# Kernel optimization log

Hardware: AMD Instinct MI355X
Metric: run time of the kernel (lower is better)

## Reference

```python
import jax, jax.numpy as jnp
import numpy as np

T, N, F, H = 8, 2048, 128, 4  # seq_len, max_nodes, hidden_dim, num_heads


def setup_inputs() -> dict:
    key = jax.random.key(0)
    k1, k2 = jax.random.split(key)
    x = jax.random.normal(k1, (T, N, F), dtype=jnp.float32)
    # xavier_uniform with gain 1.414 over (hidden_dim, hidden_dim) fan
    limit = 1.414 * np.sqrt(6.0 / (F + F))
    W = jax.random.uniform(k2, (H, F, F), dtype=jnp.float32, minval=-limit, maxval=limit)
    return {"x": x, "W": W}


def reference(x, W):
    # x: [T, N, F] padded node embeddings (all timesteps full -> mask all True)
    # W: [H, F, F] per-head projection
    seq_len = x.shape[0]
    th = jnp.einsum('tnf,hfg->htng', x, W)          # [H, T, N, F] transformed
    q = th[:, -1]                                    # [H, N, F] query = last timestep (faithful to source loop structure)
    scores = jnp.einsum('hnf,htmf->htnm', q, th)     # [H, T, N, N]
    attn = jax.nn.softmax(scores, axis=-1)           # softmax over key nodes per (head, t2)
    s = jnp.einsum('htnm,htmf->hnf', attn, th)       # sum over t2 of attn @ transformed[t2]
    s = s / seq_len                                  # mean over the seq axis (only last slot filled)
    out = jax.nn.elu(s)                              # [H, N, F]
    return out.mean(axis=0)                          # mean over heads -> [N, F]
```

## Files before the change

kernel.cpp:

```cpp
#include <hip/hip_runtime.h>
#include <hip/hip_bf16.h>
#include <math.h>

#define T_ 8
#define N_ 2048
#define F_ 128
#define H_ 4
#define NT_ (N_ / 32)

typedef unsigned int u32;
typedef unsigned short ushort_t;
typedef float f32x16 __attribute__((ext_vector_type(16)));
typedef _Float16 f16x8 __attribute__((ext_vector_type(8)));
typedef u32 u32x4 __attribute__((ext_vector_type(4)));

__global__ __launch_bounds__(256) void k_th(const float* __restrict__ x,
                                            const float* __restrict__ W,
                                            ushort_t* __restrict__ th_hi,
                                            ushort_t* __restrict__ th_hiT) {
    const int b = blockIdx.x;
    const int h = b / (T_ * (N_ / 64));
    const int rem = b % (T_ * (N_ / 64));
    const int t = rem / (N_ / 64);
    const int n0 = (rem % (N_ / 64)) * 64;
    const int tid = threadIdx.x;
    const int lane = tid & 63;
    const int w = tid >> 6;
    const int l31 = lane & 31;
    const int h5 = lane >> 5;
    const int rh = w & 1;
    const int gh = w >> 1;

    f16x8 xh[8], xl[8];
    {
        const float* xrow = x + ((size_t)t * N_ + (n0 + rh * 32 + l31)) * F_ + h5 * 8;
        #pragma unroll
        for (int ks = 0; ks < 8; ++ks) {
            float4 v0 = *reinterpret_cast<const float4*>(xrow + ks * 16);
            float4 v1 = *reinterpret_cast<const float4*>(xrow + ks * 16 + 4);
            float vv[8] = {v0.x, v0.y, v0.z, v0.w, v1.x, v1.y, v1.z, v1.w};
            f16x8 hi, lo;
            #pragma unroll
            for (int j = 0; j < 8; ++j) {
                _Float16 hh = (_Float16)vv[j];
                hi[j] = hh;
                lo[j] = (_Float16)(vv[j] - (float)hh);
            }
            xh[ks] = hi; xl[ks] = lo;
        }
    }

    f16x8 wb0[8], wb1[8];
    {
        const float* Wb = W + (size_t)h * F_ * F_ + gh * 64 + 2 * l31;
        #pragma unroll
        for (int ks = 0; ks < 8; ++ks) {
            f16x8 b0, b1;
            #pragma unroll
            for (int j = 0; j < 8; ++j) {
                float2 wv = *reinterpret_cast<const float2*>(
                    Wb + (size_t)(ks * 16 + h5 * 8 + j) * F_);
                b0[j] = (_Float16)wv.x;
                b1[j] = (_Float16)wv.y;
            }
            wb0[ks] = b0; wb1[ks] = b1;
        }
    }

    f32x16 acc0, acc1;
    #pragma unroll
    for (int r = 0; r < 16; ++r) { acc0[r] = 0.f; acc1[r] = 0.f; }
    #pragma unroll
    for (int ks = 0; ks < 8; ++ks) {
        acc0 = __builtin_amdgcn_mfma_f32_32x32x16_f16(xh[ks], wb0[ks], acc0, 0, 0, 0);
        acc1 = __builtin_amdgcn_mfma_f32_32x32x16_f16(xh[ks], wb1[ks], acc1, 0, 0, 0);
        acc0 = __builtin_amdgcn_mfma_f32_32x32x16_f16(xl[ks], wb0[ks], acc0, 0, 0, 0);
        acc1 = __builtin_amdgcn_mfma_f32_32x32x16_f16(xl[ks], wb1[ks], acc1, 0, 0, 0);
    }

    const size_t ht = (size_t)h * T_ + t;

    {
        ushort_t* base = th_hi + (ht * N_ + (size_t)(n0 + rh * 32)) * F_ + gh * 64 + 2 * l31;
        #pragma unroll
        for (int reg = 0; reg < 16; ++reg) {
            const int r = (reg & 3) + 8 * (reg >> 2) + 4 * h5;
            auto r2 = __builtin_amdgcn_cvt_pkrtz(acc0[reg], acc1[reg]);
            *reinterpret_cast<u32*>(base + (size_t)r * F_) = __builtin_bit_cast(u32, r2);
        }
    }

    {
        const int nc = (n0 >> 5) + rh;
        #pragma unroll
        for (int gs = 0; gs < 2; ++gs) {
            const int g = gh * 64 + 2 * l31 + gs;
            const f32x16& A = gs ? acc1 : acc0;
            ushort_t* bg = th_hiT + ((ht * (N_ / 32) + nc) * F_ + g) * 32;
            u32x4 run0, run1;
            run0.x = __builtin_bit_cast(u32, __builtin_amdgcn_cvt_pkrtz(A[0], A[1]));
            run0.y = __builtin_bit_cast(u32, __builtin_amdgcn_cvt_pkrtz(A[2], A[3]));
            run0.z = __builtin_bit_cast(u32, __builtin_amdgcn_cvt_pkrtz(A[4], A[5]));
            run0.w = __builtin_bit_cast(u32, __builtin_amdgcn_cvt_pkrtz(A[6], A[7]));
            run1.x = __builtin_bit_cast(u32, __builtin_amdgcn_cvt_pkrtz(A[8], A[9]));
            run1.y = __builtin_bit_cast(u32, __builtin_amdgcn_cvt_pkrtz(A[10], A[11]));
            run1.z = __builtin_bit_cast(u32, __builtin_amdgcn_cvt_pkrtz(A[12], A[13]));
            run1.w = __builtin_bit_cast(u32, __builtin_amdgcn_cvt_pkrtz(A[14], A[15]));
            *reinterpret_cast<u32x4*>(bg + 8 * h5) = run0;
            *reinterpret_cast<u32x4*>(bg + 16 + 8 * h5) = run1;
        }
    }
}

__global__ __launch_bounds__(256, 2) void k_attn(const ushort_t* __restrict__ th_hi,
                                                 const ushort_t* __restrict__ th_hiT,
                                                 ushort_t* __restrict__ s_part) {
    __shared__ ushort_t kh[3][32][128];
    __shared__ ushort_t vt[4][64][72];

    const int tid = threadIdx.x;
    const int lane = tid & 63;
    const int w = tid >> 6;
    const int l31 = lane & 31;
    const int h5 = lane >> 5;

    const int vid = ((blockIdx.x & 7) << 6) | (blockIdx.x >> 3);
    const int h = vid >> 7;
    const int t = (vid >> 4) & 7;
    const int qt = vid & 15;
    const int q0 = qt * 128 + w * 32;

    const size_t ht = (size_t)h * T_ + t;
    const ushort_t* Khi_g = th_hi + ht * (N_ * F_);
    const ushort_t* VT_g  = th_hiT + ht * ((N_ / 32) * F_ * 32);
    const ushort_t* Qhi_g = th_hi + ((size_t)h * T_ + (T_ - 1)) * (N_ * F_);

    f16x8 qh[8];
    {
        const _Float16 L2E = (_Float16)1.4426950408889634f;
        const ushort_t* qrh = Qhi_g + (size_t)(q0 + l31) * F_ + h5 * 8;
        #pragma unroll
        for (int ks = 0; ks < 8; ++ks) {
            f16x8 qv = *reinterpret_cast<const f16x8*>(qrh + ks * 16);
            #pragma unroll
            for (int j = 0; j < 8; ++j) qv[j] *= L2E;
            qh[ks] = qv;
        }
    }

    const int sm = tid >> 3;
    const int sfc = tid & 7;
    const int ssx = sm & 15;
    const int sg = tid >> 1;
    const int smh = (tid & 1) * 16;

    f32x16 o2[4];
    #pragma unroll
    for (int gs = 0; gs < 4; ++gs)
        #pragma unroll
        for (int r = 0; r < 16; ++r) o2[gs][r] = 0.f;

    float m_run = -3e38f, l_run = 0.f;

    uint4 sa0, sa1, sv0, sv1;
    f16x8 pa0, pa1;

    auto stage_load = [&](int mt) {
        const size_t grow = (size_t)(mt * 32 + sm) * F_ + sfc * 16;
        sa0 = *reinterpret_cast<const uint4*>(Khi_g + grow);
        sa1 = *reinterpret_cast<const uint4*>(Khi_g + grow + 8);
        const ushort_t* vsrc = VT_g + (size_t)mt * (F_ * 32) + (size_t)sg * 32 + smh;
        sv0 = *reinterpret_cast<const uint4*>(vsrc);
        sv1 = *reinterpret_cast<const uint4*>(vsrc + 8);
    };
    auto stage_write = [&](int kbuf, int vbuf) {
        *reinterpret_cast<uint4*>(&kh[kbuf][sm][((sfc * 2 + 0) ^ ssx) * 8]) = sa0;
        *reinterpret_cast<uint4*>(&kh[kbuf][sm][((sfc * 2 + 1) ^ ssx) * 8]) = sa1;
        ushort_t* vdst = &vt[vbuf][sg >> 1][(sg & 1) * 32 + smh];
        *reinterpret_cast<uint4*>(vdst) = sv0;
        *reinterpret_cast<uint4*>(vdst + 8) = sv1;
    };
    auto scores = [&](int kbuf) -> f32x16 {
        f32x16 S;
        #pragma unroll
        for (int r = 0; r < 16; ++r) S[r] = 0.f;
        __builtin_amdgcn_s_setprio(1);
        #pragma unroll
        for (int ks = 0; ks < 8; ++ks) {
            const f16x8 ah = *reinterpret_cast<const f16x8*>(
                &kh[kbuf][l31][((ks * 2 + h5) ^ (l31 & 15)) * 8]);
            S = __builtin_amdgcn_mfma_f32_32x32x16_f16(ah, qh[ks], S, 0, 0, 0);
        }
        __builtin_amdgcn_s_setprio(0);
        return S;
    };
    auto pv_apply = [&](int vbuf) {
        __builtin_amdgcn_s_setprio(1);
        #pragma unroll
        for (int gs = 0; gs < 4; ++gs) {
            const int g = gs * 32 + l31;
            const ushort_t* vrow = &vt[vbuf][g >> 1][(g & 1) * 32];
            f16x8 v0 = *reinterpret_cast<const f16x8*>(vrow + h5 * 8);
            f16x8 v1 = *reinterpret_cast<const f16x8*>(vrow + 16 + h5 * 8);
            o2[gs] = __builtin_amdgcn_mfma_f32_32x32x16_f16(v0, pa0, o2[gs], 0, 0, 0);
            o2[gs] = __builtin_amdgcn_mfma_f32_32x32x16_f16(v1, pa1, o2[gs], 0, 0, 0);
        }
        __builtin_amdgcn_s_setprio(0);
    };
    auto sm_only = [&](f32x16& S) {
        float m0 = fmaxf(fmaxf(S[0], S[1]), S[2]);
        float m1 = fmaxf(fmaxf(S[3], S[4]), S[5]);
        float m2 = fmaxf(fmaxf(S[6], S[7]), S[8]);
        float m3 = fmaxf(fmaxf(S[9], S[10]), S[11]);
        float m4 = fmaxf(fmaxf(S[12], S[13]), S[14]);
        float tm = fmaxf(fmaxf(fmaxf(m0, m1), m2), fmaxf(fmaxf(m3, m4), S[15]));
        tm = fmaxf(tm, __shfl_xor(tm, 32));

        if (__any(tm > m_run + 11.5416f)) {
            const float Mn = fmaxf(m_run, tm);
            const float alpha = exp2f(m_run - Mn);
            l_run *= alpha;
            #pragma unroll
            for (int gs = 0; gs < 4; ++gs)
                #pragma unroll
                for (int r = 0; r < 16; ++r) o2[gs][r] *= alpha;
            m_run = Mn;
        }
        float p[16];
        #pragma unroll
        for (int r = 0; r < 16; ++r) p[r] = exp2f(S[r] - m_run);
        float ts = (((p[0] + p[1]) + (p[2] + p[3])) + ((p[4] + p[5]) + (p[6] + p[7])))
                 + (((p[8] + p[9]) + (p[10] + p[11])) + ((p[12] + p[13]) + (p[14] + p[15])));
        l_run += ts;

        u32 pk[8];
        #pragma unroll
        for (int c = 0; c < 8; ++c) {
            auto r2 = __builtin_amdgcn_cvt_pkrtz(p[2 * c], p[2 * c + 1]);
            pk[c] = __builtin_bit_cast(u32, r2);
        }
        u32x4 t0, t1;
        t0.x = pk[0]; t0.y = pk[1]; t0.z = pk[2]; t0.w = pk[3];
        t1.x = pk[4]; t1.y = pk[5]; t1.z = pk[6]; t1.w = pk[7];
        pa0 = __builtin_bit_cast(f16x8, t0);
        pa1 = __builtin_bit_cast(f16x8, t1);
    };

    stage_load(0); stage_write(0, 0);
    stage_load(1); stage_write(1, 1);
    __syncthreads();
    f32x16 S_A = scores(0);

    stage_load(2);
    f32x16 S_B = scores(1);
    stage_write(2, 2);
    sm_only(S_A);
    __syncthreads();
    S_A = S_B;

    for (int p = 1; p <= NT_ - 2; ++p) {
        const bool more = (p + 2 <= NT_ - 1);
        if (more) stage_load(p + 2);
        S_B = scores((p + 1) % 3);
        pv_apply((p - 1) & 3);
        if (more) stage_write((p + 2) % 3, (p + 2) & 3);
        sm_only(S_A);
        __syncthreads();
        S_A = S_B;
    }

    pv_apply((NT_ - 2) & 3);
    sm_only(S_A);
    pv_apply((NT_ - 1) & 3);

    const float l_tot = l_run + __shfl_xor(l_run, 32);
    const float inv = 1.f / l_tot;
    ushort_t* dst = s_part + (ht * N_ + (size_t)(q0 + l31)) * F_;
    #pragma unroll
    for (int gs = 0; gs < 4; ++gs)
        #pragma unroll
        for (int rp = 0; rp < 8; ++rp) {
            const int r = rp * 2;
            const int g = gs * 32 + (r & 3) + 8 * (r >> 2) + 4 * h5;
            auto r2 = __builtin_amdgcn_cvt_pkrtz(o2[gs][r] * inv, o2[gs][r + 1] * inv);
            *reinterpret_cast<u32*>(dst + g) = __builtin_bit_cast(u32, r2);
        }
}

__global__ __launch_bounds__(256) void k_out(const ushort_t* __restrict__ s_part,
                                             float* __restrict__ out) {
    const int idx = blockIdx.x * blockDim.x + threadIdx.x;
    if (idx >= (N_ * F_) / 4) return;
    const int n = idx >> 5;
    const int g0 = (idx & 31) * 4;
    const float invT = 1.f / (float)T_;

    float acc[4] = {0.f, 0.f, 0.f, 0.f};
    #pragma unroll
    for (int h = 0; h < H_; ++h) {
        float hs[4] = {0.f, 0.f, 0.f, 0.f};
        #pragma unroll
        for (int t = 0; t < T_; ++t) {
            const ushort_t* p = s_part + ((size_t)(h * T_ + t) * N_ + n) * F_ + g0;
            uint2 od = *reinterpret_cast<const uint2*>(p);
            hs[0] += (float)__builtin_bit_cast(_Float16, (ushort_t)(od.x & 0xffff));
            hs[1] += (float)__builtin_bit_cast(_Float16, (ushort_t)(od.x >> 16));
            hs[2] += (float)__builtin_bit_cast(_Float16, (ushort_t)(od.y & 0xffff));
            hs[3] += (float)__builtin_bit_cast(_Float16, (ushort_t)(od.y >> 16));
        }
        #pragma unroll
        for (int k = 0; k < 4; ++k) {
            const float e = hs[k] * invT;
            acc[k] += (e > 0.f) ? e : (expf(e) - 1.f);
        }
    }
    float4 r = {acc[0] * 0.25f, acc[1] * 0.25f, acc[2] * 0.25f, acc[3] * 0.25f};
    *reinterpret_cast<float4*>(out + (size_t)n * F_ + g0) = r;
}

extern "C" void kernel_launch(void* const* d_in, const int* in_sizes, int n_in,
                              void* d_out, int out_size, void* d_ws, size_t ws_size,
                              hipStream_t stream) {
    const float* x = (const float*)d_in[0];
    const float* W = (const float*)d_in[1];
    float* out = (float*)d_out;

    const size_t TH = (size_t)H_ * T_ * N_ * F_;
    ushort_t* th_hi  = (ushort_t*)d_ws;
    ushort_t* th_hiT = th_hi + TH;
    ushort_t* s_part = th_hiT + TH;

    k_th<<<H_ * T_ * (N_ / 64), 256, 0, stream>>>(x, W, th_hi, th_hiT);
    k_attn<<<512, 256, 0, stream>>>(th_hi, th_hiT, s_part);
    k_out<<<(N_ * F_ / 4 + 255) / 256, 256, 0, stream>>>(s_part, out);
}
```

Before: 120.0 us.

## Load K fragments straight from global into registers, bypassing LDS staging

The K tile in the attention kernel is no longer staged through a triple-buffered shared-memory array. Each wave now loads its MFMA A-operand fragments directly from global memory into a pair of register buffers, and the main loop is unrolled by two to alternate between them. This removes the LDS writes, the swizzled LDS reads and the LDS footprint for K. In exchange, all four waves fetch the same K tile redundantly from global/L2, register pressure rises by two 8-fragment buffers, and the global load latency is only hidden by one iteration.

```diff
diff --git a/kernel.cpp b/kernel.cpp
--- a/kernel.cpp
+++ b/kernel.cpp
@@ -112,10 +112,11 @@
     }
 }
 
+struct KFrag { f16x8 f[8]; };
+
 __global__ __launch_bounds__(256, 2) void k_attn(const ushort_t* __restrict__ th_hi,
                                                  const ushort_t* __restrict__ th_hiT,
                                                  ushort_t* __restrict__ s_part) {
-    __shared__ ushort_t kh[3][32][128];
     __shared__ ushort_t vt[4][64][72];
 
     const int tid = threadIdx.x;
@@ -148,9 +149,8 @@
         }
     }
 
-    const int sm = tid >> 3;
-    const int sfc = tid & 7;
-    const int ssx = sm & 15;
+    const ushort_t* Krow = Khi_g + (size_t)l31 * F_ + h5 * 8;
+
     const int sg = tid >> 1;
     const int smh = (tid & 1) * 16;
 
@@ -162,35 +162,34 @@
 
     float m_run = -3e38f, l_run = 0.f;
 
-    uint4 sa0, sa1, sv0, sv1;
+    uint4 sv0, sv1;
     f16x8 pa0, pa1;
-
-    auto stage_load = [&](int mt) {
-        const size_t grow = (size_t)(mt * 32 + sm) * F_ + sfc * 16;
-        sa0 = *reinterpret_cast<const uint4*>(Khi_g + grow);
-        sa1 = *reinterpret_cast<const uint4*>(Khi_g + grow + 8);
+    KFrag krA, krB;
+
+    auto k_load = [&](int mt, KFrag& kr) {
+        const ushort_t* kp = Krow + (size_t)mt * (32 * F_);
+        #pragma unroll
+        for (int ks = 0; ks < 8; ++ks)
+            kr.f[ks] = *reinterpret_cast<const f16x8*>(kp + ks * 16);
+    };
+    auto v_load = [&](int mt) {
         const ushort_t* vsrc = VT_g + (size_t)mt * (F_ * 32) + (size_t)sg * 32 + smh;
         sv0 = *reinterpret_cast<const uint4*>(vsrc);
         sv1 = *reinterpret_cast<const uint4*>(vsrc + 8);
     };
-    auto stage_write = [&](int kbuf, int vbuf) {
-        *reinterpret_cast<uint4*>(&kh[kbuf][sm][((sfc * 2 + 0) ^ ssx) * 8]) = sa0;
-        *reinterpret_cast<uint4*>(&kh[kbuf][sm][((sfc * 2 + 1) ^ ssx) * 8]) = sa1;
+    auto v_write = [&](int vbuf) {
         ushort_t* vdst = &vt[vbuf][sg >> 1][(sg & 1) * 32 + smh];
         *reinterpret_cast<uint4*>(vdst) = sv0;
         *reinterpret_cast<uint4*>(vdst + 8) = sv1;
     };
-    auto scores = [&](int kbuf) -> f32x16 {
+    auto scores_r = [&](const KFrag& kr) -> f32x16 {
         f32x16 S;
         #pragma unroll
         for (int r = 0; r < 16; ++r) S[r] = 0.f;
         __builtin_amdgcn_s_setprio(1);
         #pragma unroll
-        for (int ks = 0; ks < 8; ++ks) {
-            const f16x8 ah = *reinterpret_cast<const f16x8*>(
-                &kh[kbuf][l31][((ks * 2 + h5) ^ (l31 & 15)) * 8]);
-            S = __builtin_amdgcn_mfma_f32_32x32x16_f16(ah, qh[ks], S, 0, 0, 0);
-        }
+        for (int ks = 0; ks < 8; ++ks)
+            S = __builtin_amdgcn_mfma_f32_32x32x16_f16(kr.f[ks], qh[ks], S, 0, 0, 0);
         __builtin_amdgcn_s_setprio(0);
         return S;
     };
@@ -246,27 +245,43 @@
         pa1 = __builtin_bit_cast(f16x8, t1);
     };
 
-    stage_load(0); stage_write(0, 0);
-    stage_load(1); stage_write(1, 1);
+    k_load(0, krA);
+    k_load(1, krB);
+    v_load(0); v_write(0);
+    v_load(1); v_write(1);
     __syncthreads();
-    f32x16 S_A = scores(0);
-
-    stage_load(2);
-    f32x16 S_B = scores(1);
-    stage_write(2, 2);
+    f32x16 S_A = scores_r(krA);
+
+    v_load(2);
+    k_load(2, krA);
+    f32x16 S_B = scores_r(krB);
+    v_write(2);
     sm_only(S_A);
     __syncthreads();
     S_A = S_B;
 
-    for (int p = 1; p <= NT_ - 2; ++p) {
-        const bool more = (p + 2 <= NT_ - 1);
-        if (more) stage_load(p + 2);
-        S_B = scores((p + 1) % 3);
-        pv_apply((p - 1) & 3);
-        if (more) stage_write((p + 2) % 3, (p + 2) & 3);
-        sm_only(S_A);
-        __syncthreads();
-        S_A = S_B;
+    for (int p = 1; p <= NT_ - 2; p += 2) {
+        {
+            const bool more = (p + 2 <= NT_ - 1);
+            if (more) { v_load(p + 2); k_load(p + 2, krB); }
+            S_B = scores_r(krA);
+            pv_apply((p - 1) & 3);
+            if (more) v_write((p + 2) & 3);
+            sm_only(S_A);
+            __syncthreads();
+            S_A = S_B;
+        }
+        {
+            const int q = p + 1;
+            const bool more = (q + 2 <= NT_ - 1);
+            if (more) { v_load(q + 2); k_load(q + 2, krA); }
+            S_B = scores_r(krB);
+            pv_apply((q - 1) & 3);
+            if (more) v_write((q + 2) & 3);
+            sm_only(S_A);
+            __syncthreads();
+            S_A = S_B;
+        }
     }
 
     pv_apply((NT_ - 2) & 3);
```

New measurement: 159.9 us. 33.3% more time.

## Widen attention key tile to 64 and replace triple-buffered pipeline with double buffering

Applied to the files above, without the earlier changes.

The attention kernel now processes 64 key nodes per iteration (two 32x32 score MFMA tiles) instead of 32. It uses plain double-buffered K/V shared memory in place of the 3/4-deep staggered pipeline, where scores for the next tile overlapped softmax and PV of the previous one. This halves the loop trip count and the number of block-wide barriers, and amortises the softmax max/rescale check over twice as many keys. In exchange it drops the explicit cross-iteration overlap of score MFMAs with softmax work and raises register and LDS pressure, which could hurt latency hiding at two blocks per CU.

```diff
diff --git a/kernel.cpp b/kernel.cpp
--- a/kernel.cpp
+++ b/kernel.cpp
@@ -6,7 +6,7 @@
 #define N_ 2048
 #define F_ 128
 #define H_ 4
-#define NT_ (N_ / 32)
+#define NT2_ (N_ / 64)
 
 typedef unsigned int u32;
 typedef unsigned short ushort_t;
@@ -115,8 +115,8 @@
 __global__ __launch_bounds__(256, 2) void k_attn(const ushort_t* __restrict__ th_hi,
                                                  const ushort_t* __restrict__ th_hiT,
                                                  ushort_t* __restrict__ s_part) {
-    __shared__ ushort_t kh[3][32][128];
-    __shared__ ushort_t vt[4][64][72];
+    __shared__ ushort_t kh[2][64][128];
+    __shared__ ushort_t vt[2][128][72];
 
     const int tid = threadIdx.x;
     const int lane = tid & 63;
@@ -148,8 +148,8 @@
         }
     }
 
-    const int sm = tid >> 3;
-    const int sfc = tid & 7;
+    const int sm = tid >> 2;
+    const int sfc = tid & 3;
     const int ssx = sm & 15;
     const int sg = tid >> 1;
     const int smh = (tid & 1) * 16;
@@ -162,58 +162,62 @@
 
     float m_run = -3e38f, l_run = 0.f;
 
-    uint4 sa0, sa1, sv0, sv1;
-    f16x8 pa0, pa1;
-
-    auto stage_load = [&](int mt) {
-        const size_t grow = (size_t)(mt * 32 + sm) * F_ + sfc * 16;
-        sa0 = *reinterpret_cast<const uint4*>(Khi_g + grow);
-        sa1 = *reinterpret_cast<const uint4*>(Khi_g + grow + 8);
-        const ushort_t* vsrc = VT_g + (size_t)mt * (F_ * 32) + (size_t)sg * 32 + smh;
-        sv0 = *reinterpret_cast<const uint4*>(vsrc);
-        sv1 = *reinterpret_cast<const uint4*>(vsrc + 8);
-    };
-    auto stage_write = [&](int kbuf, int vbuf) {
-        *reinterpret_cast<uint4*>(&kh[kbuf][sm][((sfc * 2 + 0) ^ ssx) * 8]) = sa0;
-        *reinterpret_cast<uint4*>(&kh[kbuf][sm][((sfc * 2 + 1) ^ ssx) * 8]) = sa1;
-        ushort_t* vdst = &vt[vbuf][sg >> 1][(sg & 1) * 32 + smh];
-        *reinterpret_cast<uint4*>(vdst) = sv0;
-        *reinterpret_cast<uint4*>(vdst + 8) = sv1;
-    };
-    auto scores = [&](int kbuf) -> f32x16 {
-        f32x16 S;
-        #pragma unroll
-        for (int r = 0; r < 16; ++r) S[r] = 0.f;
+    uint4 ka0, ka1, ka2, ka3;
+    uint4 sv0, sv1, sv2, sv3;
+    f16x8 pa0, pa1, pa2, pa3;
+
+    auto k_load = [&](int mt) {
+        const ushort_t* kp = Khi_g + (size_t)(mt * 64 + sm) * F_ + sfc * 32;
+        ka0 = *reinterpret_cast<const uint4*>(kp);
+        ka1 = *reinterpret_cast<const uint4*>(kp + 8);
+        ka2 = *reinterpret_cast<const uint4*>(kp + 16);
+        ka3 = *reinterpret_cast<const uint4*>(kp + 24);
+    };
+    auto k_write = [&](int buf) {
+        *reinterpret_cast<uint4*>(&kh[buf][sm][((sfc * 4 + 0) ^ ssx) * 8]) = ka0;
+        *reinterpret_cast<uint4*>(&kh[buf][sm][((sfc * 4 + 1) ^ ssx) * 8]) = ka1;
+        *reinterpret_cast<uint4*>(&kh[buf][sm][((sfc * 4 + 2) ^ ssx) * 8]) = ka2;
+        *reinterpret_cast<uint4*>(&kh[buf][sm][((sfc * 4 + 3) ^ ssx) * 8]) = ka3;
+    };
+    auto v_load = [&](int mt) {
+        const ushort_t* v0 = VT_g + (size_t)(2 * mt) * (F_ * 32) + (size_t)sg * 32 + smh;
+        const ushort_t* v1 = VT_g + (size_t)(2 * mt + 1) * (F_ * 32) + (size_t)sg * 32 + smh;
+        sv0 = *reinterpret_cast<const uint4*>(v0);
+        sv1 = *reinterpret_cast<const uint4*>(v0 + 8);
+        sv2 = *reinterpret_cast<const uint4*>(v1);
+        sv3 = *reinterpret_cast<const uint4*>(v1 + 8);
+    };
+    auto v_write = [&](int buf) {
+        ushort_t* d0 = &vt[buf][sg >> 1][(sg & 1) * 32 + smh];
+        ushort_t* d1 = &vt[buf][64 + (sg >> 1)][(sg & 1) * 32 + smh];
+        *reinterpret_cast<uint4*>(d0) = sv0;
+        *reinterpret_cast<uint4*>(d0 + 8) = sv1;
+        *reinterpret_cast<uint4*>(d1) = sv2;
+        *reinterpret_cast<uint4*>(d1 + 8) = sv3;
+    };
+    auto scores = [&](int buf, f32x16& S0, f32x16& S1) {
+        #pragma unroll
+        for (int r = 0; r < 16; ++r) { S0[r] = 0.f; S1[r] = 0.f; }
         __builtin_amdgcn_s_setprio(1);
         #pragma unroll
         for (int ks = 0; ks < 8; ++ks) {
-            const f16x8 ah = *reinterpret_cast<const f16x8*>(
-                &kh[kbuf][l31][((ks * 2 + h5) ^ (l31 & 15)) * 8]);
-            S = __builtin_amdgcn_mfma_f32_32x32x16_f16(ah, qh[ks], S, 0, 0, 0);
+            const int xo = ((ks * 2 + h5) ^ (l31 & 15)) * 8;
+            const f16x8 a0 = *reinterpret_cast<const f16x8*>(&kh[buf][l31][xo]);
+            const f16x8 a1 = *reinterpret_cast<const f16x8*>(&kh[buf][32 + l31][xo]);
+            S0 = __builtin_amdgcn_mfma_f32_32x32x16_f16(a0, qh[ks], S0, 0, 0, 0);
+            S1 = __builtin_amdgcn_mfma_f32_32x32x16_f16(a1, qh[ks], S1, 0, 0, 0);
         }
         __builtin_amdgcn_s_setprio(0);
-        return S;
-    };
-    auto pv_apply = [&](int vbuf) {
-        __builtin_amdgcn_s_setprio(1);
-        #pragma unroll
-        for (int gs = 0; gs < 4; ++gs) {
-            const int g = gs * 32 + l31;
-            const ushort_t* vrow = &vt[vbuf][g >> 1][(g & 1) * 32];
-            f16x8 v0 = *reinterpret_cast<const f16x8*>(vrow + h5 * 8);
-            f16x8 v1 = *reinterpret_cast<const f16x8*>(vrow + 16 + h5 * 8);
-            o2[gs] = __builtin_amdgcn_mfma_f32_32x32x16_f16(v0, pa0, o2[gs], 0, 0, 0);
-            o2[gs] = __builtin_amdgcn_mfma_f32_32x32x16_f16(v1, pa1, o2[gs], 0, 0, 0);
-        }
-        __builtin_amdgcn_s_setprio(0);
-    };
-    auto sm_only = [&](f32x16& S) {
-        float m0 = fmaxf(fmaxf(S[0], S[1]), S[2]);
-        float m1 = fmaxf(fmaxf(S[3], S[4]), S[5]);
-        float m2 = fmaxf(fmaxf(S[6], S[7]), S[8]);
-        float m3 = fmaxf(fmaxf(S[9], S[10]), S[11]);
-        float m4 = fmaxf(fmaxf(S[12], S[13]), S[14]);
-        float tm = fmaxf(fmaxf(fmaxf(m0, m1), m2), fmaxf(fmaxf(m3, m4), S[15]));
+    };
+    auto sm2 = [&](f32x16& S0, f32x16& S1) {
+        float c0 = fmaxf(S0[0], S1[0]);
+        float cm[8];
+        #pragma unroll
+        for (int r = 0; r < 8; ++r)
+            cm[r] = fmaxf(fmaxf(S0[2 * r], S1[2 * r]), fmaxf(S0[2 * r + 1], S1[2 * r + 1]));
+        float t0 = fmaxf(fmaxf(cm[0], cm[1]), cm[2]);
+        float t1 = fmaxf(fmaxf(cm[3], cm[4]), cm[5]);
+        float tm = fmaxf(fmaxf(cm[6], cm[7]), fmaxf(t0, t1));
         tm = fmaxf(tm, __shfl_xor(tm, 32));
 
         if (__any(tm > m_run + 11.5416f)) {
@@ -226,52 +230,68 @@
                 for (int r = 0; r < 16; ++r) o2[gs][r] *= alpha;
             m_run = Mn;
         }
-        float p[16];
-        #pragma unroll
-        for (int r = 0; r < 16; ++r) p[r] = exp2f(S[r] - m_run);
-        float ts = (((p[0] + p[1]) + (p[2] + p[3])) + ((p[4] + p[5]) + (p[6] + p[7])))
-                 + (((p[8] + p[9]) + (p[10] + p[11])) + ((p[12] + p[13]) + (p[14] + p[15])));
+        float p0[16], p1[16];
+        #pragma unroll
+        for (int r = 0; r < 16; ++r) {
+            p0[r] = exp2f(S0[r] - m_run);
+            p1[r] = exp2f(S1[r] - m_run);
+        }
+        float ts = 0.f;
+        #pragma unroll
+        for (int r = 0; r < 16; ++r) ts += p0[r] + p1[r];
         l_run += ts;
 
-        u32 pk[8];
+        u32 pk[16];
         #pragma unroll
         for (int c = 0; c < 8; ++c) {
-            auto r2 = __builtin_amdgcn_cvt_pkrtz(p[2 * c], p[2 * c + 1]);
+            auto r2 = __builtin_amdgcn_cvt_pkrtz(p0[2 * c], p0[2 * c + 1]);
             pk[c] = __builtin_bit_cast(u32, r2);
-        }
-        u32x4 t0, t1;
-        t0.x = pk[0]; t0.y = pk[1]; t0.z = pk[2]; t0.w = pk[3];
-        t1.x = pk[4]; t1.y = pk[5]; t1.z = pk[6]; t1.w = pk[7];
-        pa0 = __builtin_bit_cast(f16x8, t0);
-        pa1 = __builtin_bit_cast(f16x8, t1);
-    };
-
-    stage_load(0); stage_write(0, 0);
-    stage_load(1); stage_write(1, 1);
+            auto r3 = __builtin_amdgcn_cvt_pkrtz(p1[2 * c], p1[2 * c + 1]);
+            pk[8 + c] = __builtin_bit_cast(u32, r3);
+        }
+        u32x4 t0v, t1v, t2v, t3v;
+        t0v.x = pk[0]; t0v.y = pk[1]; t0v.z = pk[2]; t0v.w = pk[3];
+        t1v.x = pk[4]; t1v.y = pk[5]; t1v.z = pk[6]; t1v.w = pk[7];
+        t2v.x = pk[8]; t2v.y = pk[9]; t2v.z = pk[10]; t2v.w = pk[11];
+        t3v.x = pk[12]; t3v.y = pk[13]; t3v.z = pk[14]; t3v.w = pk[15];
+        pa0 = __builtin_bit_cast(f16x8, t0v);
+        pa1 = __builtin_bit_cast(f16x8, t1v);
+        pa2 = __builtin_bit_cast(f16x8, t2v);
+        pa3 = __builtin_bit_cast(f16x8, t3v);
+    };
+    auto pv_apply = [&](int buf) {
+        __builtin_amdgcn_s_setprio(1);
+        #pragma unroll
+        for (int gs = 0; gs < 4; ++gs) {
+            const int g = gs * 32 + l31;
+            const ushort_t* vr0 = &vt[buf][g >> 1][(g & 1) * 32];
+            const ushort_t* vr1 = &vt[buf][64 + (g >> 1)][(g & 1) * 32];
+            f16x8 v0 = *reinterpret_cast<const f16x8*>(vr0 + h5 * 8);
+            f16x8 v1 = *reinterpret_cast<const f16x8*>(vr0 + 16 + h5 * 8);
+            f16x8 v2 = *reinterpret_cast<const f16x8*>(vr1 + h5 * 8);
+            f16x8 v3 = *reinterpret_cast<const f16x8*>(vr1 + 16 + h5 * 8);
+            o2[gs] = __builtin_amdgcn_mfma_f32_32x32x16_f16(v0, pa0, o2[gs], 0, 0, 0);
+            o2[gs] = __builtin_amdgcn_mfma_f32_32x32x16_f16(v1, pa1, o2[gs], 0, 0, 0);
+            o2[gs] = __builtin_amdgcn_mfma_f32_32x32x16_f16(v2, pa2, o2[gs], 0, 0, 0);
+            o2[gs] = __builtin_amdgcn_mfma_f32_32x32x16_f16(v3, pa3, o2[gs], 0, 0, 0);
+        }
+        __builtin_amdgcn_s_setprio(0);
+    };
+
+    k_load(0); k_write(0);
+    v_load(0); v_write(0);
     __syncthreads();
-    f32x16 S_A = scores(0);
-
-    stage_load(2);
-    f32x16 S_B = scores(1);
-    stage_write(2, 2);
-    sm_only(S_A);
-    __syncthreads();
-    S_A = S_B;
-
-    for (int p = 1; p <= NT_ - 2; ++p) {
-        const bool more = (p + 2 <= NT_ - 1);
-        if (more) stage_load(p + 2);
-        S_B = scores((p + 1) % 3);
-        pv_apply((p - 1) & 3);
-        if (more) stage_write((p + 2) % 3, (p + 2) & 3);
-        sm_only(S_A);
+
+    for (int p = 0; p < NT2_; ++p) {
+        const bool more = (p + 1) < NT2_;
+        if (more) { k_load(p + 1); v_load(p + 1); }
+        f32x16 S0, S1;
+        scores(p & 1, S0, S1);
+        if (more) { k_write((p + 1) & 1); v_write((p + 1) & 1); }
+        sm2(S0, S1);
+        pv_apply(p & 1);
         __syncthreads();
-        S_A = S_B;
-    }
-
-    pv_apply((NT_ - 2) & 3);
-    sm_only(S_A);
-    pv_apply((NT_ - 1) & 3);
+    }
 
     const float l_tot = l_run + __shfl_xor(l_run, 32);
     const float inv = 1.f / l_tot;
```

New measurement: 117.0 us. 2.5% less time.

## Split attention key range in two with flash-decoding style merge

Applied to the files above, without the earlier changes.

Splits each attention block's key loop into two halves processed by separate blocks, doubling the grid to 1024. Each block writes normalized partial outputs plus per-row max and sum, and the output kernel merges the two halves with softmax rescaling before ELU and the head mean. The three-stage software pipeline is simplified to double buffering with smaller shared memory, which allows 4 blocks per CU. The goal is more parallelism and occupancy on the GPU, at the cost of extra partial-output traffic and merge work.

```diff
diff --git a/kernel.cpp b/kernel.cpp
--- a/kernel.cpp
+++ b/kernel.cpp
@@ -6,7 +6,7 @@
 #define N_ 2048
 #define F_ 128
 #define H_ 4
-#define NT_ (N_ / 32)
+#define NSPT_ 32
 
 typedef unsigned int u32;
 typedef unsigned short ushort_t;
@@ -112,11 +112,12 @@
     }
 }
 
-__global__ __launch_bounds__(256, 2) void k_attn(const ushort_t* __restrict__ th_hi,
+__global__ __launch_bounds__(256, 4) void k_attn(const ushort_t* __restrict__ th_hi,
                                                  const ushort_t* __restrict__ th_hiT,
-                                                 ushort_t* __restrict__ s_part) {
-    __shared__ ushort_t kh[3][32][128];
-    __shared__ ushort_t vt[4][64][72];
+                                                 ushort_t* __restrict__ o_norm,
+                                                 float* __restrict__ ml) {
+    __shared__ ushort_t kh[2][32][128];
+    __shared__ ushort_t vt[2][64][72];
 
     const int tid = threadIdx.x;
     const int lane = tid & 63;
@@ -124,11 +125,14 @@
     const int l31 = lane & 31;
     const int h5 = lane >> 5;
 
-    const int vid = ((blockIdx.x & 7) << 6) | (blockIdx.x >> 3);
-    const int h = vid >> 7;
-    const int t = (vid >> 4) & 7;
-    const int qt = vid & 15;
+    const int vid = ((blockIdx.x & 7) << 7) | (blockIdx.x >> 3);
+    const int h = vid >> 8;
+    const int t = (vid >> 5) & 7;
+    const int qt = (vid >> 1) & 15;
+    const int sp = vid & 1;
     const int q0 = qt * 128 + w * 32;
+    const int tb = sp * NSPT_;
+    const int pidx = ((h * 8 + t) * 16 + qt) * 2 + sp;
 
     const size_t ht = (size_t)h * T_ + t;
     const ushort_t* Khi_g = th_hi + ht * (N_ * F_);
@@ -162,25 +166,29 @@
 
     float m_run = -3e38f, l_run = 0.f;
 
-    uint4 sa0, sa1, sv0, sv1;
+    uint4 ka0, ka1, sv0, sv1;
     f16x8 pa0, pa1;
 
-    auto stage_load = [&](int mt) {
-        const size_t grow = (size_t)(mt * 32 + sm) * F_ + sfc * 16;
-        sa0 = *reinterpret_cast<const uint4*>(Khi_g + grow);
-        sa1 = *reinterpret_cast<const uint4*>(Khi_g + grow + 8);
-        const ushort_t* vsrc = VT_g + (size_t)mt * (F_ * 32) + (size_t)sg * 32 + smh;
+    auto k_load = [&](int p) {
+        const ushort_t* kp = Khi_g + (size_t)((tb + p) * 32 + sm) * F_ + sfc * 16;
+        ka0 = *reinterpret_cast<const uint4*>(kp);
+        ka1 = *reinterpret_cast<const uint4*>(kp + 8);
+    };
+    auto k_write = [&](int buf) {
+        *reinterpret_cast<uint4*>(&kh[buf][sm][((sfc * 2 + 0) ^ ssx) * 8]) = ka0;
+        *reinterpret_cast<uint4*>(&kh[buf][sm][((sfc * 2 + 1) ^ ssx) * 8]) = ka1;
+    };
+    auto v_load = [&](int p) {
+        const ushort_t* vsrc = VT_g + (size_t)(tb + p) * (F_ * 32) + (size_t)sg * 32 + smh;
         sv0 = *reinterpret_cast<const uint4*>(vsrc);
         sv1 = *reinterpret_cast<const uint4*>(vsrc + 8);
     };
-    auto stage_write = [&](int kbuf, int vbuf) {
-        *reinterpret_cast<uint4*>(&kh[kbuf][sm][((sfc * 2 + 0) ^ ssx) * 8]) = sa0;
-        *reinterpret_cast<uint4*>(&kh[kbuf][sm][((sfc * 2 + 1) ^ ssx) * 8]) = sa1;
-        ushort_t* vdst = &vt[vbuf][sg >> 1][(sg & 1) * 32 + smh];
+    auto v_write = [&](int buf) {
+        ushort_t* vdst = &vt[buf][sg >> 1][(sg & 1) * 32 + smh];
         *reinterpret_cast<uint4*>(vdst) = sv0;
         *reinterpret_cast<uint4*>(vdst + 8) = sv1;
     };
-    auto scores = [&](int kbuf) -> f32x16 {
+    auto scores = [&](int buf) -> f32x16 {
         f32x16 S;
         #pragma unroll
         for (int r = 0; r < 16; ++r) S[r] = 0.f;
@@ -188,24 +196,11 @@
         #pragma unroll
         for (int ks = 0; ks < 8; ++ks) {
             const f16x8 ah = *reinterpret_cast<const f16x8*>(
-                &kh[kbuf][l31][((ks * 2 + h5) ^ (l31 & 15)) * 8]);
+                &kh[buf][l31][((ks * 2 + h5) ^ (l31 & 15)) * 8]);
             S = __builtin_amdgcn_mfma_f32_32x32x16_f16(ah, qh[ks], S, 0, 0, 0);
         }
         __builtin_amdgcn_s_setprio(0);
         return S;
-    };
-    auto pv_apply = [&](int vbuf) {
-        __builtin_amdgcn_s_setprio(1);
-        #pragma unroll
-        for (int gs = 0; gs < 4; ++gs) {
-            const int g = gs * 32 + l31;
-            const ushort_t* vrow = &vt[vbuf][g >> 1][(g & 1) * 32];
-            f16x8 v0 = *reinterpret_cast<const f16x8*>(vrow + h5 * 8);
-            f16x8 v1 = *reinterpret_cast<const f16x8*>(vrow + 16 + h5 * 8);
-            o2[gs] = __builtin_amdgcn_mfma_f32_32x32x16_f16(v0, pa0, o2[gs], 0, 0, 0);
-            o2[gs] = __builtin_amdgcn_mfma_f32_32x32x16_f16(v1, pa1, o2[gs], 0, 0, 0);
-        }
-        __builtin_amdgcn_s_setprio(0);
     };
     auto sm_only = [&](f32x16& S) {
         float m0 = fmaxf(fmaxf(S[0], S[1]), S[2]);
@@ -245,37 +240,38 @@
         pa0 = __builtin_bit_cast(f16x8, t0);
         pa1 = __builtin_bit_cast(f16x8, t1);
     };
-
-    stage_load(0); stage_write(0, 0);
-    stage_load(1); stage_write(1, 1);
+    auto pv_apply = [&](int buf) {
+        __builtin_amdgcn_s_setprio(1);
+        #pragma unroll
+        for (int gs = 0; gs < 4; ++gs) {
+            const int g = gs * 32 + l31;
+            const ushort_t* vrow = &vt[buf][g >> 1][(g & 1) * 32];
+            f16x8 v0 = *reinterpret_cast<const f16x8*>(vrow + h5 * 8);
+            f16x8 v1 = *reinterpret_cast<const f16x8*>(vrow + 16 + h5 * 8);
+            o2[gs] = __builtin_amdgcn_mfma_f32_32x32x16_f16(v0, pa0, o2[gs], 0, 0, 0);
+            o2[gs] = __builtin_amdgcn_mfma_f32_32x32x16_f16(v1, pa1, o2[gs], 0, 0, 0);
+        }
+        __builtin_amdgcn_s_setprio(0);
+    };
+
+    k_load(0); k_write(0);
+    v_load(0); v_write(0);
     __syncthreads();
-    f32x16 S_A = scores(0);
-
-    stage_load(2);
-    f32x16 S_B = scores(1);
-    stage_write(2, 2);
-    sm_only(S_A);
-    __syncthreads();
-    S_A = S_B;
-
-    for (int p = 1; p <= NT_ - 2; ++p) {
-        const bool more = (p + 2 <= NT_ - 1);
-        if (more) stage_load(p + 2);
-        S_B = scores((p + 1) % 3);
-        pv_apply((p - 1) & 3);
-        if (more) stage_write((p + 2) % 3, (p + 2) & 3);
-        sm_only(S_A);
+
+    for (int p = 0; p < NSPT_; ++p) {
+        const bool more = (p + 1) < NSPT_;
+        if (more) { k_load(p + 1); v_load(p + 1); }
+        f32x16 S = scores(p & 1);
+        if (more) { k_write((p + 1) & 1); v_write((p + 1) & 1); }
+        sm_only(S);
+        pv_apply(p & 1);
         __syncthreads();
-        S_A = S_B;
-    }
-
-    pv_apply((NT_ - 2) & 3);
-    sm_only(S_A);
-    pv_apply((NT_ - 1) & 3);
+    }
 
     const float l_tot = l_run + __shfl_xor(l_run, 32);
     const float inv = 1.f / l_tot;
-    ushort_t* dst = s_part + (ht * N_ + (size_t)(q0 + l31)) * F_;
+    const int qin = w * 32 + l31;
+    ushort_t* ob = o_norm + (size_t)pidx * (128 * 128) + (size_t)qin * 128;
     #pragma unroll
     for (int gs = 0; gs < 4; ++gs)
         #pragma unroll
@@ -283,16 +279,22 @@
             const int r = rp * 2;
             const int g = gs * 32 + (r & 3) + 8 * (r >> 2) + 4 * h5;
             auto r2 = __builtin_amdgcn_cvt_pkrtz(o2[gs][r] * inv, o2[gs][r + 1] * inv);
-            *reinterpret_cast<u32*>(dst + g) = __builtin_bit_cast(u32, r2);
-        }
+            *reinterpret_cast<u32*>(ob + g) = __builtin_bit_cast(u32, r2);
+        }
+    if (h5 == 0) {
+        ml[(size_t)pidx * 256 + qin] = m_run;
+        ml[(size_t)pidx * 256 + 128 + qin] = l_tot;
+    }
 }
 
-__global__ __launch_bounds__(256) void k_out(const ushort_t* __restrict__ s_part,
+__global__ __launch_bounds__(256) void k_out(const ushort_t* __restrict__ o_norm,
+                                             const float* __restrict__ ml,
                                              float* __restrict__ out) {
     const int idx = blockIdx.x * blockDim.x + threadIdx.x;
-    if (idx >= (N_ * F_) / 4) return;
     const int n = idx >> 5;
     const int g0 = (idx & 31) * 4;
+    const int qt = n >> 7;
+    const int qin = n & 127;
     const float invT = 1.f / (float)T_;
 
     float acc[4] = {0.f, 0.f, 0.f, 0.f};
@@ -301,12 +303,26 @@
         float hs[4] = {0.f, 0.f, 0.f, 0.f};
         #pragma unroll
         for (int t = 0; t < T_; ++t) {
-            const ushort_t* p = s_part + ((size_t)(h * T_ + t) * N_ + n) * F_ + g0;
-            uint2 od = *reinterpret_cast<const uint2*>(p);
-            hs[0] += (float)__builtin_bit_cast(_Float16, (ushort_t)(od.x & 0xffff));
-            hs[1] += (float)__builtin_bit_cast(_Float16, (ushort_t)(od.x >> 16));
-            hs[2] += (float)__builtin_bit_cast(_Float16, (ushort_t)(od.y & 0xffff));
-            hs[3] += (float)__builtin_bit_cast(_Float16, (ushort_t)(od.y >> 16));
+            const size_t base2 = (size_t)((h * 8 + t) * 16 + qt) * 2;
+            const float m0 = ml[(base2 + 0) * 256 + qin];
+            const float l0 = ml[(base2 + 0) * 256 + 128 + qin];
+            const float m1 = ml[(base2 + 1) * 256 + qin];
+            const float l1 = ml[(base2 + 1) * 256 + 128 + qin];
+            const float M = fmaxf(m0, m1);
+            const float w0 = l0 * exp2f(m0 - M);
+            const float w1 = l1 * exp2f(m1 - M);
+            const float invW = 1.f / (w0 + w1);
+            const float c0 = w0 * invW, c1 = w1 * invW;
+            #pragma unroll
+            for (int s = 0; s < 2; ++s) {
+                const float cs = s ? c1 : c0;
+                uint2 od = *reinterpret_cast<const uint2*>(
+                    o_norm + (base2 + s) * (128 * 128) + (size_t)qin * 128 + g0);
+                hs[0] += cs * (float)__builtin_bit_cast(_Float16, (ushort_t)(od.x & 0xffff));
+                hs[1] += cs * (float)__builtin_bit_cast(_Float16, (ushort_t)(od.x >> 16));
+                hs[2] += cs * (float)__builtin_bit_cast(_Float16, (ushort_t)(od.y & 0xffff));
+                hs[3] += cs * (float)__builtin_bit_cast(_Float16, (ushort_t)(od.y >> 16));
+            }
         }
         #pragma unroll
         for (int k = 0; k < 4; ++k) {
@@ -326,11 +342,13 @@
     float* out = (float*)d_out;
 
     const size_t TH = (size_t)H_ * T_ * N_ * F_;
+    const size_t NPART = (size_t)H_ * T_ * 16 * 2;
     ushort_t* th_hi  = (ushort_t*)d_ws;
     ushort_t* th_hiT = th_hi + TH;
-    ushort_t* s_part = th_hiT + TH;
+    ushort_t* o_norm = th_hiT + TH;
+    float* ml = (float*)(o_norm + NPART * 128 * 128);
 
     k_th<<<H_ * T_ * (N_ / 64), 256, 0, stream>>>(x, W, th_hi, th_hiT);
-    k_attn<<<512, 256, 0, stream>>>(th_hi, th_hiT, s_part);
-    k_out<<<(N_ * F_ / 4 + 255) / 256, 256, 0, stream>>>(s_part, out);
+    k_attn<<<1024, 256, 0, stream>>>(th_hi, th_hiT, o_norm, ml);
+    k_out<<<(N_ * 32) / 256, 256, 0, stream>>>(o_norm, ml, out);
 }
```

After: 220.2 us. 83.6% more time.
